# Optimization experiments

Hardware: AMD Instinct MI355X
Metric: run time of the kernel (lower is better)

## Reference

```python
import jax, jax.numpy as jnp
import numpy as np

NUM_ATOMS = 100000
NUM_BONDS = 200000
MAX_NB = 6
ATOM_FDIM = 133
BOND_FDIM = 147
HIDDEN = 300
DEPTH = 4
NUM_MOLS = 8192


def setup_inputs() -> dict:
    key = jax.random.key(0)
    ks = jax.random.split(key, 10)
    f_atoms = jax.random.normal(ks[0], (NUM_ATOMS, ATOM_FDIM), dtype=jnp.float32)
    f_bonds = jax.random.normal(ks[1], (NUM_BONDS, BOND_FDIM), dtype=jnp.float32)
    a2b = jax.random.randint(ks[2], (NUM_ATOMS, MAX_NB), 0, NUM_BONDS, dtype=jnp.int32)
    b2a = jax.random.randint(ks[3], (NUM_BONDS,), 0, NUM_ATOMS, dtype=jnp.int32)
    b2revb = jax.random.randint(ks[4], (NUM_BONDS,), 0, NUM_BONDS, dtype=jnp.int32)
    mol_ids = jnp.sort(jax.random.randint(ks[5], (NUM_ATOMS,), 0, NUM_MOLS, dtype=jnp.int32))
    s = 1.0 / np.sqrt(HIDDEN)
    W_i = jax.random.uniform(ks[6], (BOND_FDIM, HIDDEN), jnp.float32, -s, s)
    W_h = jax.random.uniform(ks[7], (HIDDEN, HIDDEN), jnp.float32, -s, s)
    W_o = jax.random.uniform(ks[8], (ATOM_FDIM + HIDDEN, HIDDEN), jnp.float32, -s, s)
    b_o = jax.random.uniform(ks[9], (HIDDEN,), jnp.float32, -s, s)
    return {"f_atoms": f_atoms, "f_bonds": f_bonds, "W_i": W_i, "W_h": W_h,
            "W_o": W_o, "b_o": b_o, "a2b": a2b, "b2a": b2a, "b2revb": b2revb,
            "mol_ids": mol_ids}


def reference(f_atoms, f_bonds, W_i, W_h, W_o, b_o, a2b, b2a, b2revb, mol_ids):
    # initial bond messages: W_i then activation (bias=False)
    inp = f_bonds @ W_i                       # [B, H]
    message = jax.nn.relu(inp)
    for _ in range(DEPTH - 1):
        nei = message[a2b]                    # [A, MAX_NB, H] gather
        a_message = nei.sum(axis=1)           # [A, H]
        rev_message = message[b2revb]         # [B, H]
        message = a_message[b2a] - rev_message
        message = jax.nn.relu(inp + message @ W_h)
    # final atom readout
    a_message = message[a2b].sum(axis=1)      # [A, H]
    a_input = jnp.concatenate([f_atoms, a_message], axis=1)
    atom_hiddens = jax.nn.relu(a_input @ W_o + b_o)
    # per-molecule mean aggregation (== chemprop a_scope loop with 'mean')
    sums = jax.ops.segment_sum(atom_hiddens, mol_ids, num_segments=NUM_MOLS)
    counts = jax.ops.segment_sum(jnp.ones((NUM_ATOMS,), jnp.float32), mol_ids,
                                 num_segments=NUM_MOLS)
    return sums / jnp.maximum(counts, 1.0)[:, None]
```

## Files before the change

kernel.cpp:

```cpp
#include <hip/hip_runtime.h>


#define DEVFN static __device__ __forceinline__

typedef __attribute__((ext_vector_type(8))) __bf16 bf16x8;
typedef __attribute__((ext_vector_type(4))) float floatx4;

DEVFN unsigned short f2bf(float f) {
    unsigned int u = __float_as_uint(f);
    u += 0x7FFFu + ((u >> 16) & 1u);
    return (unsigned short)(u >> 16);
}
DEVFN float bf2f(unsigned int u) { return __uint_as_float(u << 16); }

DEVFN unsigned int bfsub2(unsigned int a, unsigned int m) {
    float lo = bf2f(a & 0xffffu) - bf2f(m & 0xffffu);
    float hi = bf2f(a >> 16) - bf2f(m >> 16);
    return (unsigned int)f2bf(lo) | ((unsigned int)f2bf(hi) << 16);
}

DEVFN void gll(const unsigned short* g, void* l) {
    __builtin_amdgcn_global_load_lds(
        (const __attribute__((address_space(1))) unsigned int*)g,
        (__attribute__((address_space(3))) unsigned int*)l, 16, 0, 0);
}

__global__ __launch_bounds__(256) void dbg_fill(float* out, int n, float v) {
    int t = blockIdx.x * 256 + threadIdx.x;
    if (t < n) out[t] = v;
}

__global__ __launch_bounds__(256) void prep_wih(const float* __restrict__ Wi,
                                                const float* __restrict__ Wh,
                                                unsigned short* __restrict__ Wt) {
    int t = blockIdx.x * 256 + threadIdx.x;
    if (t >= 320 * 480) return;
    int n = t / 480, k = t - n * 480;
    float v = 0.f;
    if (n < 300) {
        if (k < 147) v = Wi[k * 300 + n];
        else if (k >= 160 && k < 460) v = Wh[(k - 160) * 300 + n];
    }
    Wt[t] = f2bf(v);
}

__global__ __launch_bounds__(256) void prep_wto(const float* __restrict__ Wo,
                                                unsigned short* __restrict__ Wt) {
    int t = blockIdx.x * 256 + threadIdx.x;
    if (t >= 320 * 448) return;
    int n = t / 448, k = t - n * 448;
    float v = 0.f;
    if (n < 300) {
        if (k < 300) v = Wo[(133 + k) * 300 + n];
        else if (k >= 304 && k < 437) v = Wo[(k - 304) * 300 + n];
    }
    Wt[t] = f2bf(v);
}

__global__ __launch_bounds__(256) void pad_bonds(const float* __restrict__ fb,
                                                 unsigned short* __restrict__ out) {
    int t = blockIdx.x * 256 + threadIdx.x;
    if (t >= 200000 * 20) return;
    int b = t / 20, c = t - b * 20;
    unsigned int o[4];
#pragma unroll
    for (int p = 0; p < 4; ++p) {
        int sc = c * 8 + p * 2;
        float v0 = (sc < 147) ? fb[(size_t)b * 147 + sc] : 0.f;
        float v1 = (sc + 1 < 147) ? fb[(size_t)b * 147 + sc + 1] : 0.f;
        o[p] = (unsigned int)f2bf(v0) | ((unsigned int)f2bf(v1) << 16);
    }
    *(uint4*)(out + (size_t)b * 160 + c * 8) = make_uint4(o[0], o[1], o[2], o[3]);
}

__global__ __launch_bounds__(256) void atoms_concat(const float* __restrict__ fa,
                                                    unsigned short* __restrict__ concat) {
    int t = blockIdx.x * 256 + threadIdx.x;
    if (t >= 100000 * 18) return;
    int a = t / 18, c = t - a * 18;
    unsigned int o[4];
#pragma unroll
    for (int p = 0; p < 4; ++p) {
        int sc = c * 8 + p * 2;
        float v0 = (sc < 133) ? fa[(size_t)a * 133 + sc] : 0.f;
        float v1 = (sc + 1 < 133) ? fa[(size_t)a * 133 + sc + 1] : 0.f;
        o[p] = (unsigned int)f2bf(v0) | ((unsigned int)f2bf(v1) << 16);
    }
    *(uint4*)(concat + (size_t)a * 448 + 304 + c * 8) = make_uint4(o[0], o[1], o[2], o[3]);
}

template <int CH>
__global__ __launch_bounds__(256) void gather_sum(const unsigned short* __restrict__ msg,
                                                  const int* __restrict__ a2b,
                                                  unsigned short* __restrict__ out,
                                                  int ostride, int nA) {
    int t = blockIdx.x * 256 + threadIdx.x;
    if (t >= nA * CH) return;
    int a = t / CH, c = t - a * CH;
    float s[8] = {0, 0, 0, 0, 0, 0, 0, 0};
#pragma unroll
    for (int j = 0; j < 6; ++j) {
        int b = a2b[a * 6 + j];
        uint4 v = *(const uint4*)(msg + (size_t)b * 320 + c * 8);
        s[0] += bf2f(v.x & 0xffffu); s[1] += bf2f(v.x >> 16);
        s[2] += bf2f(v.y & 0xffffu); s[3] += bf2f(v.y >> 16);
        s[4] += bf2f(v.z & 0xffffu); s[5] += bf2f(v.z >> 16);
        s[6] += bf2f(v.w & 0xffffu); s[7] += bf2f(v.w >> 16);
    }
    unsigned int o[4];
#pragma unroll
    for (int p = 0; p < 4; ++p)
        o[p] = (unsigned int)f2bf(s[2 * p]) | ((unsigned int)f2bf(s[2 * p + 1]) << 16);
    *(uint4*)(out + (size_t)a * ostride + c * 8) = make_uint4(o[0], o[1], o[2], o[3]);
}

__global__ __launch_bounds__(256) void combine(const unsigned short* __restrict__ amsg,
                                               const unsigned short* __restrict__ msg,
                                               const int* __restrict__ b2a,
                                               const int* __restrict__ b2revb,
                                               unsigned short* __restrict__ out) {
    int t = blockIdx.x * 256 + threadIdx.x;
    if (t >= 200000 * 40) return;
    int b = t / 40, c = t - b * 40;
    int sa = b2a[b], rb = b2revb[b];
    uint4 va = *(const uint4*)(amsg + (size_t)sa * 320 + c * 8);
    uint4 vm = *(const uint4*)(msg + (size_t)rb * 320 + c * 8);
    uint4 o = make_uint4(bfsub2(va.x, vm.x), bfsub2(va.y, vm.y),
                         bfsub2(va.z, vm.z), bfsub2(va.w, vm.w));
    *(uint4*)(out + (size_t)b * 320 + c * 8) = o;
}

template <int KT0, int KT1, int MODE, int BSTRIDE>
__global__ __launch_bounds__(256) void gemm_k(const unsigned short* __restrict__ A0,
                                              int a0s,
                                              const unsigned short* __restrict__ A1,
                                              int a1s,
                                              const unsigned short* __restrict__ Wt,
                                              unsigned short* __restrict__ outp,
                                              float* __restrict__ hid,
                                              const float* __restrict__ bo, int M) {
    constexpr int KT = KT0 + KT1;
    __shared__ char lds[2 * 8192 + 2 * 10240];
    char* As = lds;
    char* Bs = lds + 16384;

    const int tid = threadIdx.x;
    const int lane = tid & 63;
    const int w = tid >> 6;
    const int wm = w & 1, wn = w >> 1;
    const int l16 = lane & 15, quad = lane >> 4;
    const int m0 = blockIdx.x * 128;
    const int n0 = blockIdx.y * 160;

    const int qg = ((tid & 3) ^ (tid >> 2) ^ (tid >> 4)) & 3;
    const int r0i = tid >> 2;
    const int gr0 = min(m0 + r0i, M - 1);
    const int gr1 = min(m0 + 64 + r0i, M - 1);
    const unsigned short* pA0a = A0 + (size_t)gr0 * a0s + qg * 8;
    const unsigned short* pA0b = A0 + (size_t)gr1 * a0s + qg * 8;
    const unsigned short* pA1a = (KT1 > 0) ? A1 + (size_t)gr0 * a1s + qg * 8 : A0;
    const unsigned short* pA1b = (KT1 > 0) ? A1 + (size_t)gr1 * a1s + qg * 8 : A0;
    const unsigned short* pB0 = Wt + (size_t)(n0 + r0i) * BSTRIDE + qg * 8;
    const unsigned short* pB1 = Wt + (size_t)(n0 + 64 + r0i) * BSTRIDE + qg * 8;
    const unsigned short* pB2 = (tid < 128)
        ? Wt + (size_t)(n0 + 128 + r0i) * BSTRIDE + qg * 8 : Wt;

    const int wl = w * 1024;

    auto issue = [&](int kt, int buf) {
        char* ab = As + buf * 8192;
        char* bb = Bs + buf * 10240;
        if (kt < KT0) {
            gll(pA0a + kt * 32, ab + wl);
            gll(pA0b + kt * 32, ab + 4096 + wl);
        } else {
            gll(pA1a + (kt - KT0) * 32, ab + wl);
            gll(pA1b + (kt - KT0) * 32, ab + 4096 + wl);
        }
        gll(pB0 + kt * 32, bb + wl);
        gll(pB1 + kt * 32, bb + 4096 + wl);
        if (tid < 128) gll(pB2 + kt * 32, bb + 8192 + wl);
    };

    const int swz = ((quad ^ l16 ^ (l16 >> 2)) & 3) * 16;
    int aoff[4], boff[5];
#pragma unroll
    for (int tm = 0; tm < 4; ++tm)
        aoff[tm] = (wm * 64 + tm * 16 + l16) * 64 + swz;
#pragma unroll
    for (int tn = 0; tn < 5; ++tn)
        boff[tn] = (wn * 80 + tn * 16 + l16) * 64 + swz;

    floatx4 acc[4][5];
#pragma unroll
    for (int tm = 0; tm < 4; ++tm)
#pragma unroll
        for (int tn = 0; tn < 5; ++tn) acc[tm][tn] = (floatx4){0.f, 0.f, 0.f, 0.f};

    issue(0, 0);
    __syncthreads();

#pragma unroll
    for (int kt = 0; kt < KT; ++kt) {
        const int buf = kt & 1;
        if (kt + 1 < KT) issue(kt + 1, buf ^ 1);

        const char* ap = As + buf * 8192;
        const char* bp = Bs + buf * 10240;
        bf16x8 av[4];
#pragma unroll
        for (int tm = 0; tm < 4; ++tm)
            av[tm] = *(const bf16x8*)(ap + aoff[tm]);
#pragma unroll
        for (int tn = 0; tn < 5; ++tn) {
            bf16x8 bv = *(const bf16x8*)(bp + boff[tn]);
#pragma unroll
            for (int tm = 0; tm < 4; ++tm)
                acc[tm][tn] = __builtin_amdgcn_mfma_f32_16x16x32_bf16(av[tm], bv, acc[tm][tn], 0, 0, 0);
        }
        __syncthreads();
    }

    float bias[5];
    if (MODE == 2) {
#pragma unroll
        for (int tn = 0; tn < 5; ++tn) {
            int col = n0 + wn * 80 + tn * 16 + l16;
            bias[tn] = (col < 300) ? bo[col] : 0.f;
        }
    }
#pragma unroll
    for (int tm = 0; tm < 4; ++tm) {
        const int r0 = m0 + wm * 64 + tm * 16 + quad * 4;
#pragma unroll
        for (int tn = 0; tn < 5; ++tn) {
            const int col = n0 + wn * 80 + tn * 16 + l16;
#pragma unroll
            for (int i = 0; i < 4; ++i) {
                int r = r0 + i;
                if (r >= M) continue;
                float c = acc[tm][tn][i];
                if (MODE == 2) {
                    if (col < 300) hid[(size_t)r * 300 + col] = fmaxf(c + bias[tn], 0.f);
                } else {
                    outp[(size_t)r * 320 + col] = f2bf(fmaxf(c, 0.f));
                }
            }
        }
    }
}

__global__ __launch_bounds__(320) void mean_k(const float* __restrict__ hid,
                                              const int* __restrict__ mol_ids,
                                              float* __restrict__ out, int nA) {
    int mol = blockIdx.x;
    int lo, hi;
    {
        int l = 0, h = nA;
        while (l < h) { int m = (l + h) >> 1; if (mol_ids[m] < mol) l = m + 1; else h = m; }
        lo = l;
    }
    {
        int l = lo, h = nA;
        while (l < h) { int m = (l + h) >> 1; if (mol_ids[m] < mol + 1) l = m + 1; else h = m; }
        hi = l;
    }
    int col = threadIdx.x;
    if (col >= 300) return;
    float s = 0.f;
    for (int a = lo; a < hi; ++a) s += hid[(size_t)a * 300 + col];
    int cnt = hi - lo;
    out[(size_t)mol * 300 + col] = s / (float)(cnt > 0 ? cnt : 1);
}

extern "C" void kernel_launch(void* const* d_in, const int* in_sizes, int n_in,
                              void* d_out, int out_size, void* d_ws, size_t ws_size,
                              hipStream_t stream) {
    (void)in_sizes; (void)n_in;
    const float* f_atoms = (const float*)d_in[0];
    const float* f_bonds = (const float*)d_in[1];
    const float* W_i     = (const float*)d_in[2];
    const float* W_h     = (const float*)d_in[3];
    const float* W_o     = (const float*)d_in[4];
    const float* b_o     = (const float*)d_in[5];
    const int*   a2b     = (const int*)d_in[6];
    const int*   b2a     = (const int*)d_in[7];
    const int*   b2revb  = (const int*)d_in[8];
    const int*   mol_ids = (const int*)d_in[9];

    const size_t sz_wih  = 320ull * 480 * 2;
    const size_t sz_wto  = 320ull * 448 * 2;
    const size_t sz_fbp  = 200000ull * 160 * 2;
    const size_t sz_amsg = 100000ull * 320 * 2;
    const size_t sz_msg  = 200000ull * 320 * 2;
    const size_t need = sz_wih + sz_wto + sz_fbp + sz_amsg + 2 * sz_msg;

    if (ws_size < need) {
        dbg_fill<<<(out_size + 255) / 256, 256, 0, stream>>>(
            (float*)d_out, out_size, (float)(ws_size >> 20));
        return;
    }

    char* ws = (char*)d_ws;
    unsigned short* wih  = (unsigned short*)(ws);
    unsigned short* wto  = (unsigned short*)(ws + sz_wih);
    unsigned short* fbp  = (unsigned short*)(ws + sz_wih + sz_wto);
    unsigned short* amsg = (unsigned short*)(ws + sz_wih + sz_wto + sz_fbp);
    unsigned short* msgA = (unsigned short*)(ws + sz_wih + sz_wto + sz_fbp + sz_amsg);
    unsigned short* msgB = (unsigned short*)(ws + sz_wih + sz_wto + sz_fbp + sz_amsg + sz_msg);
    unsigned short* concat = msgB;
    float*          hid    = (float*)fbp;

    prep_wih<<<600, 256, 0, stream>>>(W_i, W_h, wih);
    prep_wto<<<560, 256, 0, stream>>>(W_o, wto);
    pad_bonds<<<15625, 256, 0, stream>>>(f_bonds, fbp);

    gemm_k<5, 0, 0, 480><<<dim3(1563, 2), 256, 0, stream>>>(
        fbp, 160, nullptr, 0, wih, msgA, nullptr, nullptr, 200000);

    for (int d = 0; d < 3; ++d) {
        gather_sum<40><<<15625, 256, 0, stream>>>(msgA, a2b, amsg, 320, 100000);
        combine<<<31250, 256, 0, stream>>>(amsg, msgA, b2a, b2revb, msgB);
        gemm_k<5, 10, 0, 480><<<dim3(1563, 2), 256, 0, stream>>>(
            fbp, 160, msgB, 320, wih, msgA, nullptr, nullptr, 200000);
    }

    gather_sum<38><<<14844, 256, 0, stream>>>(msgA, a2b, concat, 448, 100000);
    atoms_concat<<<7032, 256, 0, stream>>>(f_atoms, concat);
    gemm_k<14, 0, 2, 448><<<dim3(782, 2), 256, 0, stream>>>(
        concat, 448, nullptr, 0, wto, nullptr, hid, b_o, 100000);
    mean_k<<<8192, 320, 0, stream>>>(hid, mol_ids, (float*)d_out, 100000);
}
```

Measured before the change: 1.285 ms.

## Use per-wave private LDS staging for A and load B directly into registers

The GEMM no longer shares A/B tiles in LDS across the block. Each wave now stages its own 64 A rows in a private LDS buffer, while the B fragments are loaded straight from global memory into registers, double-buffered. Block-wide __syncthreads barriers are replaced by per-wave s_waitcnt on vmcnt, which removes cross-wave synchronisation stalls. The cost is redundant global traffic: A rows are loaded by both waves that share wm, and B by the waves that share wn. The hand-coded waitcnt encodings are also fragile.

```diff
diff --git a/kernel.cpp b/kernel.cpp
--- a/kernel.cpp
+++ b/kernel.cpp
@@ -140,9 +140,7 @@
                                               float* __restrict__ hid,
                                               const float* __restrict__ bo, int M) {
     constexpr int KT = KT0 + KT1;
-    __shared__ char lds[2 * 8192 + 2 * 10240];
-    char* As = lds;
-    char* Bs = lds + 16384;
+    __shared__ char As[4][2][4096];
 
     const int tid = threadIdx.x;
     const int lane = tid & 63;
@@ -152,73 +150,72 @@
     const int m0 = blockIdx.x * 128;
     const int n0 = blockIdx.y * 160;
 
-    const int qg = ((tid & 3) ^ (tid >> 2) ^ (tid >> 4)) & 3;
-    const int r0i = tid >> 2;
-    const int gr0 = min(m0 + r0i, M - 1);
-    const int gr1 = min(m0 + 64 + r0i, M - 1);
-    const unsigned short* pA0a = A0 + (size_t)gr0 * a0s + qg * 8;
-    const unsigned short* pA0b = A0 + (size_t)gr1 * a0s + qg * 8;
-    const unsigned short* pA1a = (KT1 > 0) ? A1 + (size_t)gr0 * a1s + qg * 8 : A0;
-    const unsigned short* pA1b = (KT1 > 0) ? A1 + (size_t)gr1 * a1s + qg * 8 : A0;
-    const unsigned short* pB0 = Wt + (size_t)(n0 + r0i) * BSTRIDE + qg * 8;
-    const unsigned short* pB1 = Wt + (size_t)(n0 + 64 + r0i) * BSTRIDE + qg * 8;
-    const unsigned short* pB2 = (tid < 128)
-        ? Wt + (size_t)(n0 + 128 + r0i) * BSTRIDE + qg * 8 : Wt;
-
-    const int wl = w * 1024;
-
-    auto issue = [&](int kt, int buf) {
-        char* ab = As + buf * 8192;
-        char* bb = Bs + buf * 10240;
-        if (kt < KT0) {
-            gll(pA0a + kt * 32, ab + wl);
-            gll(pA0b + kt * 32, ab + 4096 + wl);
-        } else {
-            gll(pA1a + (kt - KT0) * 32, ab + wl);
-            gll(pA1b + (kt - KT0) * 32, ab + 4096 + wl);
+    const int rl = lane >> 2;
+    const int pl = lane & 3;
+    const unsigned short* pA0[4];
+    const unsigned short* pA1[4];
+#pragma unroll
+    for (int i = 0; i < 4; ++i) {
+        int r = i * 16 + rl;
+        int q = pl ^ ((r ^ (r >> 2)) & 3);
+        int gr = min(m0 + wm * 64 + r, M - 1);
+        pA0[i] = A0 + (size_t)gr * a0s + q * 8;
+        pA1[i] = (KT1 > 0) ? A1 + (size_t)gr * a1s + q * 8 : A0;
+    }
+    const unsigned short* pB[5];
+#pragma unroll
+    for (int tn = 0; tn < 5; ++tn)
+        pB[tn] = Wt + (size_t)(n0 + wn * 80 + tn * 16 + l16) * BSTRIDE + quad * 8;
+
+    const int key = (l16 ^ (l16 >> 2)) & 3;
+    int aoff[4];
+#pragma unroll
+    for (int tm = 0; tm < 4; ++tm)
+        aoff[tm] = (tm * 16 + l16) * 64 + ((quad ^ key) & 3) * 16;
+
+    floatx4 acc[4][5];
+#pragma unroll
+    for (int tm = 0; tm < 4; ++tm)
+#pragma unroll
+        for (int tn = 0; tn < 5; ++tn) acc[tm][tn] = (floatx4){0.f, 0.f, 0.f, 0.f};
+
+    bf16x8 bv[2][5];
+
+    auto issueA = [&](int kt, int st) {
+        char* dst = As[w][st];
+#pragma unroll
+        for (int i = 0; i < 4; ++i) {
+            if (kt < KT0) gll(pA0[i] + kt * 32, dst + i * 1024);
+            else          gll(pA1[i] + (kt - KT0) * 32, dst + i * 1024);
         }
-        gll(pB0 + kt * 32, bb + wl);
-        gll(pB1 + kt * 32, bb + 4096 + wl);
-        if (tid < 128) gll(pB2 + kt * 32, bb + 8192 + wl);
     };
 
-    const int swz = ((quad ^ l16 ^ (l16 >> 2)) & 3) * 16;
-    int aoff[4], boff[5];
-#pragma unroll
-    for (int tm = 0; tm < 4; ++tm)
-        aoff[tm] = (wm * 64 + tm * 16 + l16) * 64 + swz;
-#pragma unroll
-    for (int tn = 0; tn < 5; ++tn)
-        boff[tn] = (wn * 80 + tn * 16 + l16) * 64 + swz;
-
-    floatx4 acc[4][5];
-#pragma unroll
-    for (int tm = 0; tm < 4; ++tm)
-#pragma unroll
-        for (int tn = 0; tn < 5; ++tn) acc[tm][tn] = (floatx4){0.f, 0.f, 0.f, 0.f};
-
-    issue(0, 0);
-    __syncthreads();
+    issueA(0, 0);
+#pragma unroll
+    for (int tn = 0; tn < 5; ++tn) bv[0][tn] = *(const bf16x8*)(pB[tn]);
 
 #pragma unroll
     for (int kt = 0; kt < KT; ++kt) {
-        const int buf = kt & 1;
-        if (kt + 1 < KT) issue(kt + 1, buf ^ 1);
-
-        const char* ap = As + buf * 8192;
-        const char* bp = Bs + buf * 10240;
+        const int st = kt & 1;
+        if (kt + 1 < KT) {
+            issueA(kt + 1, st ^ 1);
+#pragma unroll
+            for (int tn = 0; tn < 5; ++tn)
+                bv[st ^ 1][tn] = *(const bf16x8*)(pB[tn] + (kt + 1) * 32);
+        }
+        if (kt + 1 < KT) __builtin_amdgcn_s_waitcnt(0xF79);
+        else             __builtin_amdgcn_s_waitcnt(0xF70);
+
+        const char* ap = As[w][st];
         bf16x8 av[4];
 #pragma unroll
         for (int tm = 0; tm < 4; ++tm)
             av[tm] = *(const bf16x8*)(ap + aoff[tm]);
 #pragma unroll
-        for (int tn = 0; tn < 5; ++tn) {
-            bf16x8 bv = *(const bf16x8*)(bp + boff[tn]);
+        for (int tn = 0; tn < 5; ++tn)
 #pragma unroll
             for (int tm = 0; tm < 4; ++tm)
-                acc[tm][tn] = __builtin_amdgcn_mfma_f32_16x16x32_bf16(av[tm], bv, acc[tm][tn], 0, 0, 0);
-        }
-        __syncthreads();
+                acc[tm][tn] = __builtin_amdgcn_mfma_f32_16x16x32_bf16(av[tm], bv[st][tn], acc[tm][tn], 0, 0, 0);
     }
 
     float bias[5];
```

New measurement: 1.500 ms. 1.17x slower.
